# Optimization experiments

Hardware: AMD Instinct MI355X
Metric: run time of the kernel (lower is better)

Reference implementation:

```python
import jax, jax.numpy as jnp
import numpy as np

N, E = 20000, 320000
ND, PD, HD, H = 128, 64, 128, 4
EPS = 1e-5


def gelu(x):
    return jax.nn.gelu(x, approximate=False)  # torch nn.GELU default (erf)


def setup_inputs() -> dict:
    key = jax.random.key(0)
    ks = iter(jax.random.split(key, 64))

    def lin(din, dout):
        w = jax.random.normal(next(ks), (din, dout), jnp.float32) / np.float32(np.sqrt(din))
        b = jnp.zeros((dout,), jnp.float32)
        return w, b

    inp = {}
    inp['s'] = jax.random.normal(next(ks), (N, ND), jnp.float32)
    inp['z'] = jax.random.normal(next(ks), (E, PD), jnp.float32)
    inp['edge_idx'] = jax.random.randint(next(ks), (2, E), 0, N, jnp.int32)
    # attn_weight_mlp: (2*ND+PD)->HD->HD->H
    inp['w_w1'], inp['w_b1'] = lin(2 * ND + PD, HD)
    inp['w_w2'], inp['w_b2'] = lin(HD, HD)
    inp['w_w3'], inp['w_b3'] = lin(HD, H)
    # attn_value_mlp: (ND+PD)->HD->HD->ND
    inp['v_w1'], inp['v_b1'] = lin(ND + PD, HD)
    inp['v_w2'], inp['v_b2'] = lin(HD, HD)
    inp['v_w3'], inp['v_b3'] = lin(HD, ND)
    # attn_output_linear: (HD*H)->ND + BN(ND)
    inp['o_w'], inp['o_b'] = lin(HD * H, ND)
    inp['o_g'] = jnp.ones((ND,), jnp.float32); inp['o_bb'] = jnp.zeros((ND,), jnp.float32)
    inp['o_m'] = jnp.zeros((ND,), jnp.float32); inp['o_v'] = jnp.ones((ND,), jnp.float32)
    # attn_FFN: ND->HD->ND + BN(ND)
    inp['f_w1'], inp['f_b1'] = lin(ND, HD)
    inp['f_w2'], inp['f_b2'] = lin(HD, ND)
    inp['f_g'] = jnp.ones((ND,), jnp.float32); inp['f_bb'] = jnp.zeros((ND,), jnp.float32)
    inp['f_m'] = jnp.zeros((ND,), jnp.float32); inp['f_v'] = jnp.ones((ND,), jnp.float32)
    # edge_FFN: (2*ND+PD)->HD->PD + BN(PD)
    inp['e_w1'], inp['e_b1'] = lin(2 * ND + PD, HD)
    inp['e_w2'], inp['e_b2'] = lin(HD, PD)
    inp['e_g'] = jnp.ones((PD,), jnp.float32); inp['e_bb'] = jnp.zeros((PD,), jnp.float32)
    inp['e_m'] = jnp.zeros((PD,), jnp.float32); inp['e_v'] = jnp.ones((PD,), jnp.float32)
    return inp


def reference(s, z, edge_idx,
              w_w1, w_b1, w_w2, w_b2, w_w3, w_b3,
              v_w1, v_b1, v_w2, v_b2, v_w3, v_b3,
              o_w, o_b, o_g, o_bb, o_m, o_v,
              f_w1, f_b1, f_w2, f_b2, f_g, f_bb, f_m, f_v,
              e_w1, e_b1, e_w2, e_b2, e_g, e_bb, e_m, e_v):
    # Eval mode: Dropout = identity, SyncBatchNorm uses running stats.
    src, dst = edge_idx[0], edge_idx[1]

    def bn(x, g, b, m, v):
        return (x - m) * jax.lax.rsqrt(v + EPS) * g + b

    ss, sd = s[src], s[dst]  # [E,ND] gathers
    # edge FFN residual update of z (updated z feeds attention, as in torch)
    h = gelu(jnp.concatenate([ss, sd, z], axis=1) @ e_w1 + e_b1)
    z = z + bn(h @ e_w2 + e_b2, e_g, e_bb, e_m, e_v)
    # per-edge attention logits [E,H]
    h = gelu(jnp.concatenate([sd, ss, z], axis=1) @ w_w1 + w_b1)
    h = gelu(h @ w_w2 + w_b2)
    aw = h @ w_w3 + w_b3
    # per-edge values [E,ND]
    h = gelu(jnp.concatenate([ss, z], axis=1) @ v_w1 + v_b1)
    h = gelu(h @ v_w2 + v_b2)
    av = h @ v_w3 + v_b3
    # segment softmax over incoming edges of each dst node
    mx = jax.ops.segment_max(aw, dst, num_segments=N)
    ew = jnp.exp(aw - mx[dst])
    den = jax.ops.segment_sum(ew, dst, num_segments=N)
    aw = ew / den[dst]  # [E,H]
    # weighted scatter-sum: [N,H,ND] -> flatten
    ao = jax.ops.segment_sum(aw[:, :, None] * av[:, None, :], dst, num_segments=N)
    ao = ao.reshape(N, H * ND)
    s = s + bn(ao @ o_w + o_b, o_g, o_bb, o_m, o_v)
    s = s + bn(gelu(s @ f_w1 + f_b1) @ f_w2 + f_b2, f_g, f_bb, f_m, f_v)
    return (s, z)
```

## Files before the change

### kernel.cpp

```cpp
#include <hip/hip_runtime.h>
#include <stdint.h>


#define NN 20000
#define NE 320000
#define USE_GLOAD 1

typedef unsigned short u16;
typedef __attribute__((ext_vector_type(8))) short bf16x8;
typedef __attribute__((ext_vector_type(4))) float f32x4;

__device__ __forceinline__ float bf2f(u16 u){ union{unsigned i; float f;} v; v.i=((unsigned)u)<<16; return v.f; }
__device__ __forceinline__ u16 f2bf(float f){ union{float f; unsigned i;} v; v.f=f; unsigned r = v.i + 0x7FFFu + ((v.i>>16)&1u); return (u16)(r>>16); }
__device__ __forceinline__ unsigned pk2(float a, float b){ return (unsigned)f2bf(a) | ((unsigned)f2bf(b)<<16); }
__device__ __forceinline__ float gelu_f(float x){ return 0.5f*x*(1.f+erff(x*0.70710678118654752f)); }

typedef __attribute__((address_space(3))) unsigned int as3_uint;
typedef const __attribute__((address_space(1))) unsigned int as1_uint;
__device__ __forceinline__ void gld_lds16(const void* g, void* l){
#if USE_GLOAD
  __builtin_amdgcn_global_load_lds((as1_uint*)(uintptr_t)g,
                                   (as3_uint*)(unsigned int)(uintptr_t)l, 16, 0, 0);
#endif
}

#define WT_E1 0
#define WT_E2 40960
#define WT_W1 49152
#define WT_W2 90112
#define WT_W3 106496
#define WT_V1 108544
#define WT_V2 133120
#define WT_V3 149504
#define WT_O  165888
#define WT_F1 231424
#define WT_F2 247808
#define WT_TOT 264192
#define AW_B  ((size_t)WT_TOT*2)
#define AV_B  (AW_B + (size_t)NE*16)
#define AO_B  (AV_B + (size_t)NE*256)
#define CNT_B (AO_B + (size_t)NN*1024)
#define CUR_B (CNT_B + (size_t)NN*4)
#define STA_B (CUR_B + (size_t)NN*4)
#define ORD_B (STA_B + (size_t)(NN+1)*4 + 4)

struct PrepArgs { const float* src[11]; u16* dst; };

__global__ void prep_kernel(PrepArgs A){
  const int NSrc[11] = {128,64,128,128,4,128,128,128,128,128,128};
  const int NOut[11] = {128,64,128,128,16,128,128,128,128,128,128};
  const int OFF[12]  = {0,40960,49152,90112,106496,108544,133120,149504,165888,231424,247808,264192};
  for (int g = blockIdx.x*blockDim.x + threadIdx.x; g < WT_TOT; g += gridDim.x*blockDim.x){
    int m = 0;
#pragma unroll
    for (int q=0;q<11;q++) if (g >= OFF[q+1]) m = q+1;
    int rel = g - OFF[m];
    int no = NOut[m], ns = NSrc[m];
    int c = rel/(no*64); int r2 = rel - c*no*64; int n = r2>>6; int kk = r2&63;
    int k = c*64 + kk;
    u16 v = (n < ns) ? f2bf(A.src[m][(size_t)k*ns + n]) : (u16)0;
    A.dst[OFF[m] + c*no*64 + ((n*64+kk) ^ ((n&7)<<3))] = v;
  }
}

__global__ void zero_kernel(int* c){ int i = blockIdx.x*256+threadIdx.x; if (i<NN) c[i]=0; }
__global__ void hist_kernel(const int* __restrict__ ei, int* __restrict__ cnt){
  int e = blockIdx.x*256+threadIdx.x; if (e<NE) atomicAdd(&cnt[ei[NE+e]], 1);
}
__global__ void scan_kernel(const int* __restrict__ cnt, int* __restrict__ sta, int* __restrict__ cur){
  __shared__ int part[1024];
  const int t = threadIdx.x;
  const int base = t*20;
  int s = 0;
  for (int i=0;i<20;i++){ int idx=base+i; s += (idx<NN)?cnt[idx]:0; }
  part[t]=s; __syncthreads();
  for (int off=1; off<1024; off<<=1){
    int v = (t>=off)? part[t-off] : 0;
    __syncthreads();
    part[t] += v;
    __syncthreads();
  }
  int run = part[t] - s;
  for (int i=0;i<20;i++){ int idx=base+i; if (idx<NN){ int c=cnt[idx]; sta[idx]=run; cur[idx]=run; run+=c; } }
  if (t==1023) sta[NN] = part[1023];
}
__global__ void place_kernel(const int* __restrict__ ei, int* __restrict__ cur, int* __restrict__ ord){
  int e = blockIdx.x*256+threadIdx.x;
  if (e<NE){ int p = atomicAdd(&cur[ei[NE+e]], 1); ord[p]=e; }
}

template<int NCH, int NT, int MTT, int NACC>
__device__ __forceinline__ void run_gemm(int tid, int wave, int lane,
    const u16* const (&cb)[NCH], const int (&cs)[NCH], const int (&ck)[NCH],
    const u16* __restrict__ wtG, u16* WT, f32x4 (&acc)[NACC],
    int& ntile, int& mt0, bool& active)
{
  const int lr = lane & 15, lg = lane >> 4;
  active = true;
  if (NT == 8){ ntile = wave; mt0 = 0; }
  else if (NT == 4){ ntile = wave & 3; mt0 = (wave >> 2) * NACC; }
  else { ntile = 0; mt0 = wave; active = (wave < MTT); }
  f32x4 z4 = {0.f,0.f,0.f,0.f};
#pragma unroll
  for (int m=0;m<NACC;m++) acc[m] = z4;
  const int chunkElems = NT*16*64;
#pragma unroll
  for (int c=0;c<NCH;c++){
    __syncthreads();
    const u16* src = wtG + c*chunkElems;
#if USE_GLOAD
    for (int s = wave; s < NT*2; s += 8)
      gld_lds16((const char*)src + s*1024 + lane*16, (char*)WT + s*1024);
#else
    for (int v = tid; v < chunkElems/8; v += 512)
      *(uint4*)((char*)WT + v*16) = *(const uint4*)((const char*)src + v*16);
#endif
    __syncthreads();
    const int n = ntile*16 + lr;
#pragma unroll
    for (int ks=0; ks<2; ks++){
      bf16x8 b = *(const bf16x8*)(WT + ((n*64 + ks*32 + lg*8) ^ ((n&7)<<3)));
      if (active){
#pragma unroll
        for (int m=0;m<NACC;m++){
          const u16* ap = cb[c] + ((mt0+m)*16 + lr)*cs[c] + ck[c] + ks*32 + lg*8;
          bf16x8 a = *(const bf16x8*)ap;
          acc[m] = __builtin_amdgcn_mfma_f32_16x16x32_bf16(a, b, acc[m], 0, 0, 0);
        }
      }
    }
  }
  __syncthreads();
}

template<int NACC>
__device__ __forceinline__ void epi_hb(const f32x4 (&acc)[NACC], int mt0, int ntile, int lg, int lr,
    const float* __restrict__ biasG, u16* dst, int dstride, bool act)
{
  const int col = ntile*16 + lr;
  const float b = biasG[col];
#pragma unroll
  for (int m=0;m<NACC;m++)
#pragma unroll
    for (int j=0;j<4;j++){
      int row = (mt0+m)*16 + lg*4 + j;
      float v = acc[m][j] + b;
      if (act) v = gelu_f(v);
      dst[row*dstride + col] = f2bf(v);
    }
}

struct EdgeArgs {
  const float *s, *z; const int* ei;
  const float *wb1,*wb2,*wb3,*vb1,*vb2,*vb3,*eb1,*eb2,*eg,*ebb,*em,*ev;
  const u16* wt; float* aw; u16* av; float* zout;
};

__global__ __launch_bounds__(512,4) void edge_kernel(EdgeArgs A){
  __shared__ __align__(16) u16 SS[64*136];
  __shared__ __align__(16) u16 SD[64*136];
  __shared__ __align__(16) u16 ZB[64*72];
  __shared__ __align__(16) u16 HB[64*136];
  __shared__ __align__(16) u16 WT[128*64];
  const int tid = threadIdx.x, wave = tid>>6, lane = tid&63;
  const int lg = lane>>4, lr = lane&15;
  const int e0 = blockIdx.x*64;
  {
    const int r = tid>>3, p = tid&7;
    const int sn = A.ei[e0 + r];
    const int dn = A.ei[NE + e0 + r];
    const float4* gs = (const float4*)(A.s + (size_t)sn*128 + p*16);
    float4 f0=gs[0], f1=gs[1], f2=gs[2], f3=gs[3];
    *(uint4*)(SS + r*136 + p*16)     = make_uint4(pk2(f0.x,f0.y),pk2(f0.z,f0.w),pk2(f1.x,f1.y),pk2(f1.z,f1.w));
    *(uint4*)(SS + r*136 + p*16 + 8) = make_uint4(pk2(f2.x,f2.y),pk2(f2.z,f2.w),pk2(f3.x,f3.y),pk2(f3.z,f3.w));
    const float4* gd = (const float4*)(A.s + (size_t)dn*128 + p*16);
    f0=gd[0]; f1=gd[1]; f2=gd[2]; f3=gd[3];
    *(uint4*)(SD + r*136 + p*16)     = make_uint4(pk2(f0.x,f0.y),pk2(f0.z,f0.w),pk2(f1.x,f1.y),pk2(f1.z,f1.w));
    *(uint4*)(SD + r*136 + p*16 + 8) = make_uint4(pk2(f2.x,f2.y),pk2(f2.z,f2.w),pk2(f3.x,f3.y),pk2(f3.z,f3.w));
    const float4* gz = (const float4*)(A.z + (size_t)(e0+r)*64 + p*8);
    float4 z0=gz[0], z1=gz[1];
    *(uint4*)(ZB + r*72 + p*8) = make_uint4(pk2(z0.x,z0.y),pk2(z0.z,z0.w),pk2(z1.x,z1.y),pk2(z1.z,z1.w));
  }
  int ntile, mt0; bool act_;
  {
    const u16* cb[5] = {SS,SS,SD,SD,ZB}; const int cs[5]={136,136,136,136,72}; const int ck[5]={0,64,0,64,0};
    f32x4 acc[4];
    run_gemm<5,8,4,4>(tid,wave,lane,cb,cs,ck, A.wt+WT_E1, WT, acc, ntile, mt0, act_);
    epi_hb<4>(acc, mt0, ntile, lg, lr, A.eb1, HB, 136, true);
  }
  {
    const u16* cb[2] = {HB,HB}; const int cs[2]={136,136}; const int ck[2]={0,64};
    f32x4 acc[2];
    run_gemm<2,4,4,2>(tid,wave,lane,cb,cs,ck, A.wt+WT_E2, WT, acc, ntile, mt0, act_);
    const int col = ntile*16 + lr;
    const float b  = A.eb2[col];
    const float sc = A.eg[col] * rsqrtf(A.ev[col] + 1e-5f);
    const float sh = A.ebb[col] - A.em[col]*sc;
#pragma unroll
    for (int m=0;m<2;m++)
#pragma unroll
      for (int j=0;j<4;j++){
        int row = (mt0+m)*16 + lg*4 + j;
        float zo = A.z[(size_t)(e0+row)*64 + col];
        float zn = zo + (acc[m][j]+b)*sc + sh;
        A.zout[(size_t)(e0+row)*64 + col] = zn;
        ZB[row*72 + col] = f2bf(zn);
      }
  }
  {
    const u16* cb[5] = {SD,SD,SS,SS,ZB}; const int cs[5]={136,136,136,136,72}; const int ck[5]={0,64,0,64,0};
    f32x4 acc[4];
    run_gemm<5,8,4,4>(tid,wave,lane,cb,cs,ck, A.wt+WT_W1, WT, acc, ntile, mt0, act_);
    epi_hb<4>(acc, mt0, ntile, lg, lr, A.wb1, HB, 136, true);
  }
  {
    const u16* cb[2] = {HB,HB}; const int cs[2]={136,136}; const int ck[2]={0,64};
    f32x4 acc[4];
    run_gemm<2,8,4,4>(tid,wave,lane,cb,cs,ck, A.wt+WT_W2, WT, acc, ntile, mt0, act_);
    epi_hb<4>(acc, mt0, ntile, lg, lr, A.wb2, HB, 136, true);
  }
  {
    const u16* cb[2] = {HB,HB}; const int cs[2]={136,136}; const int ck[2]={0,64};
    f32x4 acc[1];
    run_gemm<2,1,4,1>(tid,wave,lane,cb,cs,ck, A.wt+WT_W3, WT, acc, ntile, mt0, act_);
    if (act_ && lr < 4){
      const float b = A.wb3[lr];
#pragma unroll
      for (int j=0;j<4;j++){
        int row = mt0*16 + lg*4 + j;
        A.aw[(size_t)(e0+row)*4 + lr] = acc[0][j] + b;
      }
    }
  }
  {
    const u16* cb[3] = {SS,SS,ZB}; const int cs[3]={136,136,72}; const int ck[3]={0,64,0};
    f32x4 acc[4];
    run_gemm<3,8,4,4>(tid,wave,lane,cb,cs,ck, A.wt+WT_V1, WT, acc, ntile, mt0, act_);
    epi_hb<4>(acc, mt0, ntile, lg, lr, A.vb1, HB, 136, true);
  }
  {
    const u16* cb[2] = {HB,HB}; const int cs[2]={136,136}; const int ck[2]={0,64};
    f32x4 acc[4];
    run_gemm<2,8,4,4>(tid,wave,lane,cb,cs,ck, A.wt+WT_V2, WT, acc, ntile, mt0, act_);
    epi_hb<4>(acc, mt0, ntile, lg, lr, A.vb2, HB, 136, true);
  }
  {
    const u16* cb[2] = {HB,HB}; const int cs[2]={136,136}; const int ck[2]={0,64};
    f32x4 acc[4];
    run_gemm<2,8,4,4>(tid,wave,lane,cb,cs,ck, A.wt+WT_V3, WT, acc, ntile, mt0, act_);
    epi_hb<4>(acc, mt0, ntile, lg, lr, A.vb3, HB, 136, false);
    __syncthreads();
    { const int r = tid>>3, p = tid&7;
      uint4 v0 = *(const uint4*)(HB + r*136 + p*16);
      uint4 v1 = *(const uint4*)(HB + r*136 + p*16 + 8);
      *(uint4*)(A.av + (size_t)(e0+r)*128 + p*16) = v0;
      *(uint4*)(A.av + (size_t)(e0+r)*128 + p*16 + 8) = v1; }
  }
}

__global__ void attn_kernel(const float* __restrict__ aw, const u16* __restrict__ av,
                            const int* __restrict__ sta, const int* __restrict__ ord,
                            u16* __restrict__ ao){
  const int node = blockIdx.x; const int t = threadIdx.x;
  const int b = sta[node], e = sta[node+1];
  float m0=-3.4e38f, m1=m0, m2=m0, m3=m0;
  for (int i=b;i<e;i++){
    int ed = ord[i]; float4 a = *(const float4*)(aw + (size_t)ed*4);
    m0=fmaxf(m0,a.x); m1=fmaxf(m1,a.y); m2=fmaxf(m2,a.z); m3=fmaxf(m3,a.w);
  }
  float d0=0,d1=0,d2=0,d3=0,a0=0,a1=0,a2=0,a3=0;
  for (int i=b;i<e;i++){
    int ed = ord[i]; float4 a = *(const float4*)(aw + (size_t)ed*4);
    float w0=__expf(a.x-m0), w1=__expf(a.y-m1), w2=__expf(a.z-m2), w3=__expf(a.w-m3);
    d0+=w0; d1+=w1; d2+=w2; d3+=w3;
    float v = bf2f(av[(size_t)ed*128 + t]);
    a0 += w0*v; a1 += w1*v; a2 += w2*v; a3 += w3*v;
  }
  size_t o = (size_t)node*512 + t;
  if (e > b){
    ao[o      ] = f2bf(a0/d0);
    ao[o + 128] = f2bf(a1/d1);
    ao[o + 256] = f2bf(a2/d2);
    ao[o + 384] = f2bf(a3/d3);
  } else {
    ao[o] = 0; ao[o+128] = 0; ao[o+256] = 0; ao[o+384] = 0;
  }
}

struct NodeArgs {
  const float* s; const u16* ao; const u16* wt;
  const float *ob,*og,*obb,*om,*ov,*fb1,*fb2,*fg,*fbb,*fm,*fv;
  float* outS;
};

__global__ __launch_bounds__(512,4) void node_kernel(NodeArgs A){
  __shared__ __align__(16) u16 AO[16*520];
  __shared__ __align__(16) u16 WT[128*64];
  __shared__ __align__(16) float S1F[16*128];
  __shared__ __align__(16) u16 S1B[16*136];
  __shared__ __align__(16) u16 HB2[16*136];
  const int tid=threadIdx.x, wave=tid>>6, lane=tid&63;
  const int lg=lane>>4, lr=lane&15;
  const int n0 = blockIdx.x*16;
  { const int r=tid>>5, p=tid&31;
    const uint4* gp = (const uint4*)(A.ao + (size_t)(n0+r)*512 + p*16);
    uint4 v0=gp[0], v1=gp[1];
    *(uint4*)(AO + r*520 + p*16) = v0;
    *(uint4*)(AO + r*520 + p*16 + 8) = v1;
  }
  int ntile, mt0; bool act_;
  float sc, sh, bb;
  {
    const u16* cb[8]={AO,AO,AO,AO,AO,AO,AO,AO};
    const int cs[8]={520,520,520,520,520,520,520,520};
    const int ck[8]={0,64,128,192,256,320,384,448};
    f32x4 acc[1];
    run_gemm<8,8,1,1>(tid,wave,lane,cb,cs,ck, A.wt+WT_O, WT, acc, ntile, mt0, act_);
    const int col = wave*16+lr;
    bb = A.ob[col];
    sc = A.og[col] * rsqrtf(A.ov[col] + 1e-5f);
    sh = A.obb[col] - A.om[col]*sc;
#pragma unroll
    for (int j=0;j<4;j++){
      int row = lg*4+j;
      float so = A.s[(size_t)(n0+row)*128 + col];
      float s1 = so + (acc[0][j]+bb)*sc + sh;
      S1F[row*128+col] = s1;
      S1B[row*136+col] = f2bf(s1);
    }
  }
  {
    const u16* cb[2]={S1B,S1B}; const int cs[2]={136,136}; const int ck[2]={0,64};
    f32x4 acc[1];
    run_gemm<2,8,1,1>(tid,wave,lane,cb,cs,ck, A.wt+WT_F1, WT, acc, ntile, mt0, act_);
    epi_hb<1>(acc, 0, wave, lg, lr, A.fb1, HB2, 136, true);
  }
  {
    const u16* cb[2]={HB2,HB2}; const int cs[2]={136,136}; const int ck[2]={0,64};
    f32x4 acc[1];
    run_gemm<2,8,1,1>(tid,wave,lane,cb,cs,ck, A.wt+WT_F2, WT, acc, ntile, mt0, act_);
    const int col = wave*16+lr;
    const float b2  = A.fb2[col];
    const float sc2 = A.fg[col] * rsqrtf(A.fv[col] + 1e-5f);
    const float sh2 = A.fbb[col] - A.fm[col]*sc2;
#pragma unroll
    for (int j=0;j<4;j++){
      int row = lg*4+j;
      float v = S1F[row*128+col] + (acc[0][j]+b2)*sc2 + sh2;
      A.outS[(size_t)(n0+row)*128 + col] = v;
    }
  }
}

extern "C" void kernel_launch(void* const* d_in, const int* in_sizes, int n_in,
                              void* d_out, int out_size, void* d_ws, size_t ws_size,
                              hipStream_t stream)
{
  const float* sG = (const float*)d_in[0];
  const float* zG = (const float*)d_in[1];
  const int* eiG = (const int*)d_in[2];
  char* ws = (char*)d_ws;
  u16*  wt  = (u16*)ws;
  float* aw = (float*)(ws + AW_B);
  u16*  av  = (u16*)(ws + AV_B);
  u16*  ao  = (u16*)(ws + AO_B);
  int* cnt = (int*)(ws + CNT_B);
  int* cur = (int*)(ws + CUR_B);
  int* sta = (int*)(ws + STA_B);
  int* ord = (int*)(ws + ORD_B);
  float* outS = (float*)d_out;
  float* outZ = outS + (size_t)NN*128;

  PrepArgs P;
  const int srcIdx[11] = {29,31,3,5,7,9,11,13,15,21,23};
  for (int i=0;i<11;i++) P.src[i] = (const float*)d_in[srcIdx[i]];
  P.dst = wt;
  prep_kernel<<<dim3(1032), dim3(256), 0, stream>>>(P);
  zero_kernel<<<dim3((NN+255)/256), dim3(256), 0, stream>>>(cnt);
  hist_kernel<<<dim3((NE+255)/256), dim3(256), 0, stream>>>(eiG, cnt);
  scan_kernel<<<dim3(1), dim3(1024), 0, stream>>>(cnt, sta, cur);
  place_kernel<<<dim3((NE+255)/256), dim3(256), 0, stream>>>(eiG, cur, ord);

  EdgeArgs E;
  E.s = sG; E.z = zG; E.ei = eiG;
  E.wb1=(const float*)d_in[4];  E.wb2=(const float*)d_in[6];  E.wb3=(const float*)d_in[8];
  E.vb1=(const float*)d_in[10]; E.vb2=(const float*)d_in[12]; E.vb3=(const float*)d_in[14];
  E.eb1=(const float*)d_in[30]; E.eb2=(const float*)d_in[32];
  E.eg=(const float*)d_in[33]; E.ebb=(const float*)d_in[34]; E.em=(const float*)d_in[35]; E.ev=(const float*)d_in[36];
  E.wt = wt; E.aw = aw; E.av = av; E.zout = outZ;
  edge_kernel<<<dim3(NE/64), dim3(512), 0, stream>>>(E);

  attn_kernel<<<dim3(NN), dim3(128), 0, stream>>>(aw, av, sta, ord, ao);

  NodeArgs Nd;
  Nd.s = sG; Nd.ao = ao; Nd.wt = wt;
  Nd.ob=(const float*)d_in[16]; Nd.og=(const float*)d_in[17]; Nd.obb=(const float*)d_in[18];
  Nd.om=(const float*)d_in[19]; Nd.ov=(const float*)d_in[20];
  Nd.fb1=(const float*)d_in[22]; Nd.fb2=(const float*)d_in[24];
  Nd.fg=(const float*)d_in[25]; Nd.fbb=(const float*)d_in[26]; Nd.fm=(const float*)d_in[27]; Nd.fv=(const float*)d_in[28];
  Nd.outS = outS;
  node_kernel<<<dim3(NN/16), dim3(512), 0, stream>>>(Nd);
}
```

Baseline: 761.4 us.

## Load GEMM weights directly into registers, replace erf GELU with tanh approximation

The GEMM helper no longer stages each weight chunk into shared memory behind two block barriers. Each wave now reads its B fragments straight from global memory (unswizzled layout) and prefetches the next chunk, and ping-pong hidden buffers with explicit barriers between stages take the place of the shared buffer. GELU switches from the exact erf form to a tanh approximation built on exp and rcp, and bf16 packing uses the hardware v_cvt_pk_bf16_f32 instruction. Weight prep becomes a tiled transpose through shared memory. The tanh GELU deviates from the erf reference, which risks accuracy, and the per-wave global weight reads rely on L1/L2 hits.

New measurement: 671.0 us. -11.9%, faster.

```diff
diff --git a/kernel.cpp b/kernel.cpp
--- a/kernel.cpp
+++ b/kernel.cpp
@@ -4,7 +4,6 @@
 
 #define NN 20000
 #define NE 320000
-#define USE_GLOAD 1
 
 typedef unsigned short u16;
 typedef __attribute__((ext_vector_type(8))) short bf16x8;
@@ -12,16 +11,16 @@
 
 __device__ __forceinline__ float bf2f(u16 u){ union{unsigned i; float f;} v; v.i=((unsigned)u)<<16; return v.f; }
 __device__ __forceinline__ u16 f2bf(float f){ union{float f; unsigned i;} v; v.f=f; unsigned r = v.i + 0x7FFFu + ((v.i>>16)&1u); return (u16)(r>>16); }
-__device__ __forceinline__ unsigned pk2(float a, float b){ return (unsigned)f2bf(a) | ((unsigned)f2bf(b)<<16); }
-__device__ __forceinline__ float gelu_f(float x){ return 0.5f*x*(1.f+erff(x*0.70710678118654752f)); }
-
-typedef __attribute__((address_space(3))) unsigned int as3_uint;
-typedef const __attribute__((address_space(1))) unsigned int as1_uint;
-__device__ __forceinline__ void gld_lds16(const void* g, void* l){
-#if USE_GLOAD
-  __builtin_amdgcn_global_load_lds((as1_uint*)(uintptr_t)g,
-                                   (as3_uint*)(unsigned int)(uintptr_t)l, 16, 0, 0);
-#endif
+__device__ __forceinline__ unsigned pk2(float a, float b){
+  unsigned r; asm("v_cvt_pk_bf16_f32 %0, %1, %2" : "=v"(r) : "v"(a), "v"(b)); return r;
+}
+__device__ __forceinline__ float gelu_f(float x){
+  float y = 0.7978845608f*x*(1.0f + 0.044715f*x*x);
+  float a = fabsf(y);
+  float t = __expf(-2.0f*a);
+  float th = (1.0f - t)*__builtin_amdgcn_rcpf(1.0f + t);
+  th = copysignf(th, y);
+  return 0.5f*x*(1.0f + th);
 }
 
 #define WT_E1 0
@@ -47,19 +46,42 @@
 struct PrepArgs { const float* src[11]; u16* dst; };
 
 __global__ void prep_kernel(PrepArgs A){
-  const int NSrc[11] = {128,64,128,128,4,128,128,128,128,128,128};
-  const int NOut[11] = {128,64,128,128,16,128,128,128,128,128,128};
-  const int OFF[12]  = {0,40960,49152,90112,106496,108544,133120,149504,165888,231424,247808,264192};
-  for (int g = blockIdx.x*blockDim.x + threadIdx.x; g < WT_TOT; g += gridDim.x*blockDim.x){
-    int m = 0;
-#pragma unroll
-    for (int q=0;q<11;q++) if (g >= OFF[q+1]) m = q+1;
-    int rel = g - OFF[m];
-    int no = NOut[m], ns = NSrc[m];
-    int c = rel/(no*64); int r2 = rel - c*no*64; int n = r2>>6; int kk = r2&63;
-    int k = c*64 + kk;
-    u16 v = (n < ns) ? f2bf(A.src[m][(size_t)k*ns + n]) : (u16)0;
-    A.dst[OFF[m] + c*no*64 + ((n*64+kk) ^ ((n&7)<<3))] = v;
+  constexpr int NS[11]  = {128, 64,128,128,  4,128,128,128,128,128,128};
+  constexpr int NO[11]  = {128, 64,128,128, 16,128,128,128,128,128,128};
+  constexpr int OFF[11] = {0,40960,49152,90112,106496,108544,133120,149504,165888,231424,247808};
+  constexpr int CUM[12] = {0,10,12,22,26,28,34,38,42,58,62,66};
+  __shared__ float T[64][72];
+  const int bid = blockIdx.x, t = threadIdx.x;
+  int m = 0;
+#pragma unroll
+  for (int q=0;q<11;q++) if (bid >= CUM[q+1]) m = q+1;
+  const int rel = bid - CUM[m];
+  const int ntn = (NO[m] > 64) ? 2 : 1;
+  const int c  = rel / ntn;
+  const int nt = rel - c*ntn;
+  const float* src = A.src[m];
+  if (m != 4){
+    const int k = t>>2, q = t&3;
+    const float* sp = src + (size_t)(c*64+k)*NS[m] + nt*64 + q*16;
+    float4 v0=((const float4*)sp)[0], v1=((const float4*)sp)[1], v2=((const float4*)sp)[2], v3=((const float4*)sp)[3];
+    float* tp = &T[k][q*16];
+    ((float4*)tp)[0]=v0; ((float4*)tp)[1]=v1; ((float4*)tp)[2]=v2; ((float4*)tp)[3]=v3;
+  } else {
+    for (int lin = t; lin < 64*16; lin += 256){
+      int k = lin>>4, n = lin&15;
+      T[k][n] = (n < 4) ? src[(size_t)(c*64+k)*4 + n] : 0.f;
+    }
+  }
+  __syncthreads();
+  const int nl = t>>2, kq = (t&3)*16;
+  const int n = nt*64 + nl;
+  if (nl < 64 && n < NO[m]){
+    unsigned w[8];
+#pragma unroll
+    for (int i=0;i<8;i++) w[i] = pk2(T[kq+2*i][nl], T[kq+2*i+1][nl]);
+    u16* dp = A.dst + OFF[m] + (size_t)c*NO[m]*64 + (size_t)n*64 + kq;
+    ((uint4*)dp)[0] = make_uint4(w[0],w[1],w[2],w[3]);
+    ((uint4*)dp)[1] = make_uint4(w[4],w[5],w[6],w[7]);
   }
 }
 
@@ -90,9 +112,9 @@
 }
 
 template<int NCH, int NT, int MTT, int NACC>
-__device__ __forceinline__ void run_gemm(int tid, int wave, int lane,
+__device__ __forceinline__ void run_gemm2(int wave, int lane,
     const u16* const (&cb)[NCH], const int (&cs)[NCH], const int (&ck)[NCH],
-    const u16* __restrict__ wtG, u16* WT, f32x4 (&acc)[NACC],
+    const u16* __restrict__ wtG, f32x4 (&acc)[NACC],
     int& ntile, int& mt0, bool& active)
 {
   const int lr = lane & 15, lg = lane >> 4;
@@ -103,34 +125,28 @@
   f32x4 z4 = {0.f,0.f,0.f,0.f};
 #pragma unroll
   for (int m=0;m<NACC;m++) acc[m] = z4;
-  const int chunkElems = NT*16*64;
+  if (!active) return;
+  const int CE = NT*16*64;
+  const u16* bp = wtG + (size_t)(ntile*16+lr)*64 + lg*8;
+  bf16x8 bc0 = *(const bf16x8*)bp;
+  bf16x8 bc1 = *(const bf16x8*)(bp + 32);
 #pragma unroll
   for (int c=0;c<NCH;c++){
-    __syncthreads();
-    const u16* src = wtG + c*chunkElems;
-#if USE_GLOAD
-    for (int s = wave; s < NT*2; s += 8)
-      gld_lds16((const char*)src + s*1024 + lane*16, (char*)WT + s*1024);
-#else
-    for (int v = tid; v < chunkElems/8; v += 512)
-      *(uint4*)((char*)WT + v*16) = *(const uint4*)((const char*)src + v*16);
-#endif
-    __syncthreads();
-    const int n = ntile*16 + lr;
-#pragma unroll
-    for (int ks=0; ks<2; ks++){
-      bf16x8 b = *(const bf16x8*)(WT + ((n*64 + ks*32 + lg*8) ^ ((n&7)<<3)));
-      if (active){
-#pragma unroll
-        for (int m=0;m<NACC;m++){
-          const u16* ap = cb[c] + ((mt0+m)*16 + lr)*cs[c] + ck[c] + ks*32 + lg*8;
-          bf16x8 a = *(const bf16x8*)ap;
-          acc[m] = __builtin_amdgcn_mfma_f32_16x16x32_bf16(a, b, acc[m], 0, 0, 0);
-        }
-      }
-    }
-  }
-  __syncthreads();
+    bf16x8 bn0, bn1;
+    if (c+1 < NCH){
+      bn0 = *(const bf16x8*)(bp + (c+1)*CE);
+      bn1 = *(const bf16x8*)(bp + (c+1)*CE + 32);
+    }
+#pragma unroll
+    for (int m=0;m<NACC;m++){
+      const u16* ap = cb[c] + (size_t)((mt0+m)*16 + lr)*cs[c] + ck[c] + lg*8;
+      bf16x8 a0 = *(const bf16x8*)ap;
+      bf16x8 a1 = *(const bf16x8*)(ap + 32);
+      acc[m] = __builtin_amdgcn_mfma_f32_16x16x32_bf16(a0, bc0, acc[m], 0, 0, 0);
+      acc[m] = __builtin_amdgcn_mfma_f32_16x16x32_bf16(a1, bc1, acc[m], 0, 0, 0);
+    }
+    bc0 = bn0; bc1 = bn1;
+  }
 }
 
 template<int NACC>
@@ -159,9 +175,9 @@
 __global__ __launch_bounds__(512,4) void edge_kernel(EdgeArgs A){
   __shared__ __align__(16) u16 SS[64*136];
   __shared__ __align__(16) u16 SD[64*136];
-  __shared__ __align__(16) u16 ZB[64*72];
-  __shared__ __align__(16) u16 HB[64*136];
-  __shared__ __align__(16) u16 WT[128*64];
+  __shared__ __align__(16) u16 ZB[64*88];
+  __shared__ __align__(16) u16 HB1[64*136];
+  __shared__ __align__(16) u16 HB2[64*136];
   const int tid = threadIdx.x, wave = tid>>6, lane = tid&63;
   const int lg = lane>>4, lr = lane&15;
   const int e0 = blockIdx.x*64;
@@ -179,19 +195,21 @@
     *(uint4*)(SD + r*136 + p*16 + 8) = make_uint4(pk2(f2.x,f2.y),pk2(f2.z,f2.w),pk2(f3.x,f3.y),pk2(f3.z,f3.w));
     const float4* gz = (const float4*)(A.z + (size_t)(e0+r)*64 + p*8);
     float4 z0=gz[0], z1=gz[1];
-    *(uint4*)(ZB + r*72 + p*8) = make_uint4(pk2(z0.x,z0.y),pk2(z0.z,z0.w),pk2(z1.x,z1.y),pk2(z1.z,z1.w));
-  }
+    *(uint4*)(ZB + r*88 + p*8) = make_uint4(pk2(z0.x,z0.y),pk2(z0.z,z0.w),pk2(z1.x,z1.y),pk2(z1.z,z1.w));
+  }
+  __syncthreads();
   int ntile, mt0; bool act_;
   {
-    const u16* cb[5] = {SS,SS,SD,SD,ZB}; const int cs[5]={136,136,136,136,72}; const int ck[5]={0,64,0,64,0};
-    f32x4 acc[4];
-    run_gemm<5,8,4,4>(tid,wave,lane,cb,cs,ck, A.wt+WT_E1, WT, acc, ntile, mt0, act_);
-    epi_hb<4>(acc, mt0, ntile, lg, lr, A.eb1, HB, 136, true);
-  }
-  {
-    const u16* cb[2] = {HB,HB}; const int cs[2]={136,136}; const int ck[2]={0,64};
+    const u16* cb[5] = {SS,SS,SD,SD,ZB}; const int cs[5]={136,136,136,136,88}; const int ck[5]={0,64,0,64,0};
+    f32x4 acc[4];
+    run_gemm2<5,8,4,4>(wave,lane,cb,cs,ck, A.wt+WT_E1, acc, ntile, mt0, act_);
+    epi_hb<4>(acc, mt0, ntile, lg, lr, A.eb1, HB1, 136, true);
+  }
+  __syncthreads();
+  {
+    const u16* cb[2] = {HB1,HB1}; const int cs[2]={136,136}; const int ck[2]={0,64};
     f32x4 acc[2];
-    run_gemm<2,4,4,2>(tid,wave,lane,cb,cs,ck, A.wt+WT_E2, WT, acc, ntile, mt0, act_);
+    run_gemm2<2,4,4,2>(wave,lane,cb,cs,ck, A.wt+WT_E2, acc, ntile, mt0, act_);
     const int col = ntile*16 + lr;
     const float b  = A.eb2[col];
     const float sc = A.eg[col] * rsqrtf(A.ev[col] + 1e-5f);
@@ -204,25 +222,28 @@
         float zo = A.z[(size_t)(e0+row)*64 + col];
         float zn = zo + (acc[m][j]+b)*sc + sh;
         A.zout[(size_t)(e0+row)*64 + col] = zn;
-        ZB[row*72 + col] = f2bf(zn);
+        ZB[row*88 + col] = f2bf(zn);
       }
   }
-  {
-    const u16* cb[5] = {SD,SD,SS,SS,ZB}; const int cs[5]={136,136,136,136,72}; const int ck[5]={0,64,0,64,0};
-    f32x4 acc[4];
-    run_gemm<5,8,4,4>(tid,wave,lane,cb,cs,ck, A.wt+WT_W1, WT, acc, ntile, mt0, act_);
-    epi_hb<4>(acc, mt0, ntile, lg, lr, A.wb1, HB, 136, true);
-  }
-  {
-    const u16* cb[2] = {HB,HB}; const int cs[2]={136,136}; const int ck[2]={0,64};
-    f32x4 acc[4];
-    run_gemm<2,8,4,4>(tid,wave,lane,cb,cs,ck, A.wt+WT_W2, WT, acc, ntile, mt0, act_);
-    epi_hb<4>(acc, mt0, ntile, lg, lr, A.wb2, HB, 136, true);
-  }
-  {
-    const u16* cb[2] = {HB,HB}; const int cs[2]={136,136}; const int ck[2]={0,64};
+  __syncthreads();
+  {
+    const u16* cb[5] = {SD,SD,SS,SS,ZB}; const int cs[5]={136,136,136,136,88}; const int ck[5]={0,64,0,64,0};
+    f32x4 acc[4];
+    run_gemm2<5,8,4,4>(wave,lane,cb,cs,ck, A.wt+WT_W1, acc, ntile, mt0, act_);
+    epi_hb<4>(acc, mt0, ntile, lg, lr, A.wb1, HB2, 136, true);
+  }
+  __syncthreads();
+  {
+    const u16* cb[2] = {HB2,HB2}; const int cs[2]={136,136}; const int ck[2]={0,64};
+    f32x4 acc[4];
+    run_gemm2<2,8,4,4>(wave,lane,cb,cs,ck, A.wt+WT_W2, acc, ntile, mt0, act_);
+    epi_hb<4>(acc, mt0, ntile, lg, lr, A.wb2, HB1, 136, true);
+  }
+  __syncthreads();
+  {
+    const u16* cb[2] = {HB1,HB1}; const int cs[2]={136,136}; const int ck[2]={0,64};
     f32x4 acc[1];
-    run_gemm<2,1,4,1>(tid,wave,lane,cb,cs,ck, A.wt+WT_W3, WT, acc, ntile, mt0, act_);
+    run_gemm2<2,1,4,1>(wave,lane,cb,cs,ck, A.wt+WT_W3, acc, ntile, mt0, act_);
     if (act_ && lr < 4){
       const float b = A.wb3[lr];
 #pragma unroll
@@ -233,26 +254,28 @@
     }
   }
   {
-    const u16* cb[3] = {SS,SS,ZB}; const int cs[3]={136,136,72}; const int ck[3]={0,64,0};
-    f32x4 acc[4];
-    run_gemm<3,8,4,4>(tid,wave,lane,cb,cs,ck, A.wt+WT_V1, WT, acc, ntile, mt0, act_);
-    epi_hb<4>(acc, mt0, ntile, lg, lr, A.vb1, HB, 136, true);
-  }
-  {
-    const u16* cb[2] = {HB,HB}; const int cs[2]={136,136}; const int ck[2]={0,64};
-    f32x4 acc[4];
-    run_gemm<2,8,4,4>(tid,wave,lane,cb,cs,ck, A.wt+WT_V2, WT, acc, ntile, mt0, act_);
-    epi_hb<4>(acc, mt0, ntile, lg, lr, A.vb2, HB, 136, true);
-  }
-  {
-    const u16* cb[2] = {HB,HB}; const int cs[2]={136,136}; const int ck[2]={0,64};
-    f32x4 acc[4];
-    run_gemm<2,8,4,4>(tid,wave,lane,cb,cs,ck, A.wt+WT_V3, WT, acc, ntile, mt0, act_);
-    epi_hb<4>(acc, mt0, ntile, lg, lr, A.vb3, HB, 136, false);
+    const u16* cb[3] = {SS,SS,ZB}; const int cs[3]={136,136,88}; const int ck[3]={0,64,0};
+    f32x4 acc[4];
+    run_gemm2<3,8,4,4>(wave,lane,cb,cs,ck, A.wt+WT_V1, acc, ntile, mt0, act_);
+    epi_hb<4>(acc, mt0, ntile, lg, lr, A.vb1, HB2, 136, true);
+  }
+  __syncthreads();
+  {
+    const u16* cb[2] = {HB2,HB2}; const int cs[2]={136,136}; const int ck[2]={0,64};
+    f32x4 acc[4];
+    run_gemm2<2,8,4,4>(wave,lane,cb,cs,ck, A.wt+WT_V2, acc, ntile, mt0, act_);
+    epi_hb<4>(acc, mt0, ntile, lg, lr, A.vb2, HB1, 136, true);
+  }
+  __syncthreads();
+  {
+    const u16* cb[2] = {HB1,HB1}; const int cs[2]={136,136}; const int ck[2]={0,64};
+    f32x4 acc[4];
+    run_gemm2<2,8,4,4>(wave,lane,cb,cs,ck, A.wt+WT_V3, acc, ntile, mt0, act_);
+    epi_hb<4>(acc, mt0, ntile, lg, lr, A.vb3, HB2, 136, false);
     __syncthreads();
     { const int r = tid>>3, p = tid&7;
-      uint4 v0 = *(const uint4*)(HB + r*136 + p*16);
-      uint4 v1 = *(const uint4*)(HB + r*136 + p*16 + 8);
+      uint4 v0 = *(const uint4*)(HB2 + r*136 + p*16);
+      uint4 v1 = *(const uint4*)(HB2 + r*136 + p*16 + 8);
       *(uint4*)(A.av + (size_t)(e0+r)*128 + p*16) = v0;
       *(uint4*)(A.av + (size_t)(e0+r)*128 + p*16 + 8) = v1; }
   }
@@ -295,10 +318,9 @@
 
 __global__ __launch_bounds__(512,4) void node_kernel(NodeArgs A){
   __shared__ __align__(16) u16 AO[16*520];
-  __shared__ __align__(16) u16 WT[128*64];
   __shared__ __align__(16) float S1F[16*128];
   __shared__ __align__(16) u16 S1B[16*136];
-  __shared__ __align__(16) u16 HB2[16*136];
+  __shared__ __align__(16) u16 HBx[16*136];
   const int tid=threadIdx.x, wave=tid>>6, lane=tid&63;
   const int lg=lane>>4, lr=lane&15;
   const int n0 = blockIdx.x*16;
@@ -308,18 +330,18 @@
     *(uint4*)(AO + r*520 + p*16) = v0;
     *(uint4*)(AO + r*520 + p*16 + 8) = v1;
   }
+  __syncthreads();
   int ntile, mt0; bool act_;
-  float sc, sh, bb;
   {
     const u16* cb[8]={AO,AO,AO,AO,AO,AO,AO,AO};
     const int cs[8]={520,520,520,520,520,520,520,520};
     const int ck[8]={0,64,128,192,256,320,384,448};
     f32x4 acc[1];
-    run_gemm<8,8,1,1>(tid,wave,lane,cb,cs,ck, A.wt+WT_O, WT, acc, ntile, mt0, act_);
+    run_gemm2<8,8,1,1>(wave,lane,cb,cs,ck, A.wt+WT_O, acc, ntile, mt0, act_);
     const int col = wave*16+lr;
-    bb = A.ob[col];
-    sc = A.og[col] * rsqrtf(A.ov[col] + 1e-5f);
-    sh = A.obb[col] - A.om[col]*sc;
+    const float bb = A.ob[col];
+    const float sc = A.og[col] * rsqrtf(A.ov[col] + 1e-5f);
+    const float sh = A.obb[col] - A.om[col]*sc;
 #pragma unroll
     for (int j=0;j<4;j++){
       int row = lg*4+j;
@@ -329,16 +351,18 @@
       S1B[row*136+col] = f2bf(s1);
     }
   }
+  __syncthreads();
   {
     const u16* cb[2]={S1B,S1B}; const int cs[2]={136,136}; const int ck[2]={0,64};
     f32x4 acc[1];
-    run_gemm<2,8,1,1>(tid,wave,lane,cb,cs,ck, A.wt+WT_F1, WT, acc, ntile, mt0, act_);
-    epi_hb<1>(acc, 0, wave, lg, lr, A.fb1, HB2, 136, true);
-  }
-  {
-    const u16* cb[2]={HB2,HB2}; const int cs[2]={136,136}; const int ck[2]={0,64};
+    run_gemm2<2,8,1,1>(wave,lane,cb,cs,ck, A.wt+WT_F1, acc, ntile, mt0, act_);
+    epi_hb<1>(acc, 0, wave, lg, lr, A.fb1, HBx, 136, true);
+  }
+  __syncthreads();
+  {
+    const u16* cb[2]={HBx,HBx}; const int cs[2]={136,136}; const int ck[2]={0,64};
     f32x4 acc[1];
-    run_gemm<2,8,1,1>(tid,wave,lane,cb,cs,ck, A.wt+WT_F2, WT, acc, ntile, mt0, act_);
+    run_gemm2<2,8,1,1>(wave,lane,cb,cs,ck, A.wt+WT_F2, acc, ntile, mt0, act_);
     const int col = wave*16+lr;
     const float b2  = A.fb2[col];
     const float sc2 = A.fg[col] * rsqrtf(A.fv[col] + 1e-5f);
@@ -375,7 +399,7 @@
   const int srcIdx[11] = {29,31,3,5,7,9,11,13,15,21,23};
   for (int i=0;i<11;i++) P.src[i] = (const float*)d_in[srcIdx[i]];
   P.dst = wt;
-  prep_kernel<<<dim3(1032), dim3(256), 0, stream>>>(P);
+  prep_kernel<<<dim3(66), dim3(256), 0, stream>>>(P);
   zero_kernel<<<dim3((NN+255)/256), dim3(256), 0, stream>>>(cnt);
   hist_kernel<<<dim3((NE+255)/256), dim3(256), 0, stream>>>(eiG, cnt);
   scan_kernel<<<dim3(1), dim3(1024), 0, stream>>>(cnt, sta, cur);
```
